# Optimization experiments

Measured on AMD Instinct MI355X. Metric: run time of the kernel, lower is better.

## Reference

```python
import jax, jax.numpy as jnp
import numpy as np

D_MODEL, EDGE_DIM, HIDDEN = 128, 9, 256
B, N = 2, 512


def setup_inputs() -> dict:
    key = jax.random.key(0)
    ks = jax.random.split(key, 12)
    s = 0.05
    return {
        "z_prime": jax.random.normal(ks[0], (B, N, D_MODEL), jnp.float32),
        "edge_features": jax.random.normal(ks[1], (N, N, EDGE_DIM), jnp.float32),
        "candidate_edge_mask": jax.random.randint(ks[2], (N, N), 0, 2, jnp.int32),
        # organ head params (in, out) layout
        "Wo1": jax.random.normal(ks[3], (D_MODEL, HIDDEN), jnp.float32) * s,
        "bo1": jnp.zeros((HIDDEN,), jnp.float32),
        "Wo2": jax.random.normal(ks[4], (HIDDEN, 1), jnp.float32) * s,
        "bo2": jnp.zeros((1,), jnp.float32),
        # edge head first linear, split by input blocks [zi | zj | edge_feat]
        "We_i": jax.random.normal(ks[5], (D_MODEL, HIDDEN), jnp.float32) * s,
        "We_j": jax.random.normal(ks[6], (D_MODEL, HIDDEN), jnp.float32) * s,
        "We_e": jax.random.normal(ks[7], (EDGE_DIM, HIDDEN), jnp.float32) * s,
        "be1": jnp.zeros((HIDDEN,), jnp.float32),
        "We2": jax.random.normal(ks[8], (HIDDEN, 1), jnp.float32) * s,
        "be2": jnp.zeros((1,), jnp.float32),
    }


def reference(z_prime, edge_features, candidate_edge_mask,
              Wo1, bo1, Wo2, bo2, We_i, We_j, We_e, be1, We2, be2):
    # organ head: sigmoid(MLP(z)) -> (B, N)
    h_o = jax.nn.relu(jnp.einsum('bnd,dh->bnh', z_prime, Wo1) + bo1)
    organ_susceptibility = jax.nn.sigmoid(
        (jnp.einsum('bnh,ho->bno', h_o, Wo2) + bo2).squeeze(-1))

    # edge head: concat([zi, zj, E]) @ W1 decomposed into per-node/per-edge
    # projections (identical math to the concatenated linear).
    pi = jnp.einsum('bnd,dh->bnh', z_prime, We_i)   # (B, N, H) -> broadcast over j
    pj = jnp.einsum('bnd,dh->bnh', z_prime, We_j)   # (B, N, H) -> broadcast over i
    pe = jnp.einsum('ijd,dh->ijh', edge_features, We_e)  # (N, N, H)
    h = jax.nn.relu(pi[:, :, None, :] + pj[:, None, :, :] + pe[None] + be1)
    edge_prob = jax.nn.sigmoid(
        (jnp.einsum('bijh,ho->bijo', h, We2) + be2).squeeze(-1))
    edge_prob = edge_prob * candidate_edge_mask.astype(edge_prob.dtype)[None]
    return (organ_susceptibility, edge_prob)
```

## Files before the change

kernel.cpp:

```cpp
#include <hip/hip_runtime.h>
#include <math.h>
#include <stdint.h>

#define D_MODEL 128
#define EDGE_DIM 9
#define HIDDEN 256
#define BATCH 2
#define NN 512

typedef _Float16 h2v    __attribute__((ext_vector_type(2)));
typedef __fp16   fp16x2 __attribute__((ext_vector_type(2)));
typedef _Float16 f16x8  __attribute__((ext_vector_type(8)));
typedef float    f32x4  __attribute__((ext_vector_type(4)));

struct H8 { h2v v[4]; };

__device__ __forceinline__ uint32_t h2u(h2v v) { return __builtin_bit_cast(uint32_t, v); }
__device__ __forceinline__ h2v u2h(uint32_t u) { return __builtin_bit_cast(h2v, u); }
__device__ __forceinline__ h2v pkrtz(float a, float b) {
    return __builtin_bit_cast(h2v, __builtin_amdgcn_cvt_pkrtz(a, b));
}
__device__ __forceinline__ h2v relu2(h2v v) {
    h2v z = {(_Float16)0.0f, (_Float16)0.0f};
    return __builtin_elementwise_max(v, z);
}
__device__ __forceinline__ float fdot2(h2v a, h2v b, float c) {
    return __builtin_amdgcn_fdot2(__builtin_bit_cast(fp16x2, a),
                                  __builtin_bit_cast(fp16x2, b), c, false);
}
__device__ __forceinline__ float sigmoidf_(float x) { return 1.f / (1.f + expf(-x)); }
__device__ __forceinline__ uint32_t el(const uint4& u, int k) {
    switch (k) { case 0: return u.x; case 1: return u.y; case 2: return u.z; default: return u.w; }
}

__global__ __launch_bounds__(512) void node_mfma_kernel(
    const float* __restrict__ z,
    const float* __restrict__ Wo1,
    const float* __restrict__ bo1,
    const float* __restrict__ Wo2,
    const float* __restrict__ bo2,
    const float* __restrict__ We_i,
    const float* __restrict__ We_j,
    const float* __restrict__ be1,
    float* __restrict__ organ_out,
    uint32_t* __restrict__ pi_h,
    uint32_t* __restrict__ pj_q)
{
    __shared__ uint32_t Wlds[256][68];
    __shared__ float org_part[32][4];

    const int t    = threadIdx.x;
    const int lane = t & 63;
    const int wave = t >> 6;
    const int rb   = blockIdx.x;
    const int m    = blockIdx.y;

    const float* __restrict__ W = (m == 0) ? Wo1 : (m == 1) ? We_i : We_j;

    for (int idx = t; idx < 64 * 256; idx += 512) {
        const int d2 = idx >> 8;
        const int h  = idx & 255;
        const float wlo = W[(2 * d2) * 256 + h];
        const float whi = W[(2 * d2 + 1) * 256 + h];
        Wlds[h][d2 ^ ((h & 7) << 3)] = h2u(pkrtz(wlo, whi));
    }

    const int rt = wave & 1;
    const int cg = wave >> 1;
    const int kg = lane >> 4;
    const int row = rb * 32 + rt * 16 + (lane & 15);

    f16x8 A[4];
#pragma unroll
    for (int kt = 0; kt < 4; ++kt) {
        const float4 za = *(const float4*)&z[(size_t)row * 128 + kt * 32 + kg * 8];
        const float4 zb = *(const float4*)&z[(size_t)row * 128 + kt * 32 + kg * 8 + 4];
        H8 a;
        a.v[0] = pkrtz(za.x, za.y); a.v[1] = pkrtz(za.z, za.w);
        a.v[2] = pkrtz(zb.x, zb.y); a.v[3] = pkrtz(zb.z, zb.w);
        A[kt] = __builtin_bit_cast(f16x8, a);
    }

    __syncthreads();

    f32x4 C[4];
#pragma unroll
    for (int ct = 0; ct < 4; ++ct) {
        const int col = (cg * 4 + ct) * 16 + (lane & 15);
        C[ct] = (f32x4){0.f, 0.f, 0.f, 0.f};
#pragma unroll
        for (int kt = 0; kt < 4; ++kt) {
            const int d2b = (kt * 16 + kg * 4) ^ ((col & 7) << 3);
            const uint4 w = *(const uint4*)&Wlds[col][d2b];
            H8 b;
            b.v[0] = u2h(w.x); b.v[1] = u2h(w.y);
            b.v[2] = u2h(w.z); b.v[3] = u2h(w.w);
            C[ct] = __builtin_amdgcn_mfma_f32_16x16x32_f16(
                        A[kt], __builtin_bit_cast(f16x8, b), C[ct], 0, 0, 0);
        }
    }

    if (m == 0) {
        float s0 = 0.f, s1 = 0.f, s2 = 0.f, s3 = 0.f;
#pragma unroll
        for (int ct = 0; ct < 4; ++ct) {
            const int col = (cg * 4 + ct) * 16 + (lane & 15);
            const float b1 = bo1[col];
            const float w2 = Wo2[col];
            s0 = fmaf(fmaxf(C[ct].x + b1, 0.f), w2, s0);
            s1 = fmaf(fmaxf(C[ct].y + b1, 0.f), w2, s1);
            s2 = fmaf(fmaxf(C[ct].z + b1, 0.f), w2, s2);
            s3 = fmaf(fmaxf(C[ct].w + b1, 0.f), w2, s3);
        }
#pragma unroll
        for (int off = 1; off <= 8; off <<= 1) {
            s0 += __shfl_xor(s0, off, 64);
            s1 += __shfl_xor(s1, off, 64);
            s2 += __shfl_xor(s2, off, 64);
            s3 += __shfl_xor(s3, off, 64);
        }
        if ((lane & 15) == 0) {
            const int rbase = rt * 16 + kg * 4;
            org_part[rbase + 0][cg] = s0;
            org_part[rbase + 1][cg] = s1;
            org_part[rbase + 2][cg] = s2;
            org_part[rbase + 3][cg] = s3;
        }
        __syncthreads();
        if (t < 32) {
            const float s = org_part[t][0] + org_part[t][1]
                          + org_part[t][2] + org_part[t][3] + bo2[0];
            organ_out[rb * 32 + t] = sigmoidf_(s);
        }
    } else if (m == 1) {
#pragma unroll
        for (int ct = 0; ct < 4; ++ct) {
            const int col = (cg * 4 + ct) * 16 + (lane & 15);
            const float bv = be1[col];
            float v0 = C[ct].x + bv, v1 = C[ct].y + bv;
            float v2 = C[ct].z + bv, v3 = C[ct].w + bv;
            const float p0 = __shfl_xor(v0, 1, 64);
            const float p1 = __shfl_xor(v1, 1, 64);
            const float p2 = __shfl_xor(v2, 1, 64);
            const float p3 = __shfl_xor(v3, 1, 64);
            if (!(lane & 1)) {
                const int hp = col >> 1;
                const size_t gr = (size_t)(rb * 32 + rt * 16 + kg * 4);
                pi_h[(gr + 0) * 128 + hp] = h2u(pkrtz(v0, p0));
                pi_h[(gr + 1) * 128 + hp] = h2u(pkrtz(v1, p1));
                pi_h[(gr + 2) * 128 + hp] = h2u(pkrtz(v2, p2));
                pi_h[(gr + 3) * 128 + hp] = h2u(pkrtz(v3, p3));
            }
        }
    } else {
#pragma unroll
        for (int ct = 0; ct < 4; ++ct) {
            const int col = (cg * 4 + ct) * 16 + (lane & 15);
            float v0 = C[ct].x, v1 = C[ct].y, v2 = C[ct].z, v3 = C[ct].w;
            const float p0 = __shfl_xor(v0, 1, 64);
            const float p1 = __shfl_xor(v1, 1, 64);
            const float p2 = __shfl_xor(v2, 1, 64);
            const float p3 = __shfl_xor(v3, 1, 64);
            if (!(lane & 1)) {
                const int hp = col >> 1;
                const size_t gr = (size_t)(rb * 32 + rt * 16 + kg * 4);
                const size_t gbase = (size_t)(hp >> 2) * 1024;
                const int    sub   = hp & 3;
                pj_q[(gbase + gr + 0) * 4 + sub] = h2u(pkrtz(v0, p0));
                pj_q[(gbase + gr + 1) * 4 + sub] = h2u(pkrtz(v1, p1));
                pj_q[(gbase + gr + 2) * 4 + sub] = h2u(pkrtz(v2, p2));
                pj_q[(gbase + gr + 3) * 4 + sub] = h2u(pkrtz(v3, p3));
            }
        }
    }
}

__global__ __launch_bounds__(256) void edge_kernel(
    const float* __restrict__ E,
    const int*   __restrict__ mask,
    const float* __restrict__ We_e,
    const float* __restrict__ We2,
    const float* __restrict__ be2,
    const uint32_t* __restrict__ pi_h,
    const uint32_t* __restrict__ pj_q,
    float* __restrict__ edge_out)
{
    __shared__ __align__(16) uint32_t wee_s[EDGE_DIM][128];
    __shared__ __align__(16) uint32_t we2_s[128];
    __shared__ __align__(16) uint32_t pi_s[BATCH][8][128];

    const int t    = threadIdx.x;
    const int lane = t & 63;
    const int w    = t >> 6;
    const int bi   = blockIdx.x;
    const int i0   = (bi >> 4) * 8;
    const int j0   = (bi & 15) * 32;

    const int jl = lane & 31;
    const int ih = lane >> 5;
    const int il = 2 * w + ih;

    for (int idx = t; idx < EDGE_DIM * 128; idx += 256) {
        const int d  = idx >> 7;
        const int h2 = idx & 127;
        wee_s[d][h2] = h2u(pkrtz(We_e[d * 256 + 2 * h2], We_e[d * 256 + 2 * h2 + 1]));
    }
    if (t < 128) we2_s[t] = h2u(pkrtz(We2[2 * t], We2[2 * t + 1]));
#pragma unroll
    for (int k = 0; k < 2; ++k) {
        const int idx = t + k * 256;
        const int r16 = idx >> 5;
        const int c4  = idx & 31;
        const int b   = r16 >> 3;
        const int ii  = r16 & 7;
        const uint4 v = *(const uint4*)&pi_h[(size_t)(b * NN + i0 + ii) * 128 + c4 * 4];
        *(uint4*)&pi_s[b][ii][c4 * 4] = v;
    }

    h2v e[9];
    {
        const float* eptr = &E[((size_t)(i0 + il) * NN + j0 + jl) * EDGE_DIM];
        float ef[9];
#pragma unroll
        for (int d = 0; d < EDGE_DIM; ++d) ef[d] = eptr[d];
#pragma unroll
        for (int d = 0; d < EDGE_DIM; ++d) e[d] = pkrtz(ef[d], ef[d]);
    }

    __syncthreads();

    float acc[2] = {0.f, 0.f};

    const uint4* __restrict__ pjQ = (const uint4*)pj_q;
    const int jrow = j0 + jl;

    uint4 pjn0 = pjQ[jrow];
    uint4 pjn1 = pjQ[NN + jrow];

#pragma unroll 1
    for (int hc = 0; hc < 128; hc += 4) {
        const int g = hc >> 2;
        const uint4 pj40 = pjn0;
        const uint4 pj41 = pjn1;
        if (g < 31) {
            pjn0 = pjQ[(g + 1) * 1024 + jrow];
            pjn1 = pjQ[(g + 1) * 1024 + NN + jrow];
        }
        __builtin_amdgcn_sched_barrier(0);

        uint4 wee4[EDGE_DIM];
#pragma unroll
        for (int d = 0; d < EDGE_DIM; ++d) wee4[d] = *(const uint4*)&wee_s[d][hc];
        const uint4 we24 = *(const uint4*)&we2_s[hc];
        uint4 pi4[2];
        pi4[0] = *(const uint4*)&pi_s[0][il][hc];
        pi4[1] = *(const uint4*)&pi_s[1][il][hc];

#pragma unroll
        for (int k = 0; k < 4; ++k) {
            const h2v w2k = u2h(el(we24, k));
            h2v pe = e[0] * u2h(el(wee4[0], k));
#pragma unroll
            for (int d = 1; d < EDGE_DIM; ++d) pe += e[d] * u2h(el(wee4[d], k));
            h2v t0 = relu2(pe + u2h(el(pj40, k)) + u2h(el(pi4[0], k)));
            acc[0] = fdot2(t0, w2k, acc[0]);
            h2v t1 = relu2(pe + u2h(el(pj41, k)) + u2h(el(pi4[1], k)));
            acc[1] = fdot2(t1, w2k, acc[1]);
        }
    }

    const float b2 = be2[0];
    const int i = i0 + il;
    const float mv = (float)mask[(size_t)i * NN + j0 + jl];
#pragma unroll
    for (int b = 0; b < 2; ++b) {
        const float s = acc[b] + b2;
        edge_out[((size_t)b * NN + i) * NN + j0 + jl] = sigmoidf_(s) * mv;
    }
}

extern "C" void kernel_launch(void* const* d_in, const int* in_sizes, int n_in,
                              void* d_out, int out_size, void* d_ws, size_t ws_size,
                              hipStream_t stream) {
    const float* z    = (const float*)d_in[0];
    const float* E    = (const float*)d_in[1];
    const int*   mask = (const int*)  d_in[2];
    const float* Wo1  = (const float*)d_in[3];
    const float* bo1  = (const float*)d_in[4];
    const float* Wo2  = (const float*)d_in[5];
    const float* bo2  = (const float*)d_in[6];
    const float* We_i = (const float*)d_in[7];
    const float* We_j = (const float*)d_in[8];
    const float* We_e = (const float*)d_in[9];
    const float* be1  = (const float*)d_in[10];
    const float* We2  = (const float*)d_in[11];
    const float* be2  = (const float*)d_in[12];

    float* out_organ = (float*)d_out;
    float* out_edge  = out_organ + BATCH * NN;

    uint32_t* pi_h = (uint32_t*)d_ws;
    uint32_t* pj_q = pi_h + (size_t)BATCH * NN * (HIDDEN/2);

    hipLaunchKernelGGL(node_mfma_kernel,
                       dim3(32, 3), dim3(512), 0, stream,
                       z, Wo1, bo1, Wo2, bo2, We_i, We_j, be1,
                       out_organ, pi_h, pj_q);

    hipLaunchKernelGGL(edge_kernel,
                       dim3(64 * 16), dim3(256), 0, stream,
                       E, mask, We_e, We2, be2, pi_h, pj_q, out_edge);
}
```

Measured before the change: 37.55 us.

## Split edge kernel hidden dimension across waves with shared-memory partial reduction

Each edge block now covers 4 rows of i instead of 8, and the four waves are split into two halves that each handle half of the hidden dimension. The halves combine their partial dot products through shared memory before the sigmoid and mask. This doubles the grid size to raise parallelism and shortens each thread's serial loop. In exchange it recomputes the edge-feature projection per half, adds a barrier and shared-memory reduction, and drops the software prefetch of pj loads.

```diff
diff --git a/kernel.cpp b/kernel.cpp
--- a/kernel.cpp
+++ b/kernel.cpp
@@ -187,18 +187,19 @@
 {
     __shared__ __align__(16) uint32_t wee_s[EDGE_DIM][128];
     __shared__ __align__(16) uint32_t we2_s[128];
-    __shared__ __align__(16) uint32_t pi_s[BATCH][8][128];
+    __shared__ __align__(16) uint32_t pi_s[BATCH][4][128];
+    __shared__ __align__(16) float    part_s[4][32][2];
 
     const int t    = threadIdx.x;
     const int lane = t & 63;
     const int w    = t >> 6;
     const int bi   = blockIdx.x;
-    const int i0   = (bi >> 4) * 8;
+    const int i0   = (bi >> 4) * 4;
     const int j0   = (bi & 15) * 32;
 
     const int jl = lane & 31;
-    const int ih = lane >> 5;
-    const int il = 2 * w + ih;
+    const int il = 2 * (w & 1) + (lane >> 5);
+    const int hh = w >> 1;
 
     for (int idx = t; idx < EDGE_DIM * 128; idx += 256) {
         const int d  = idx >> 7;
@@ -206,13 +207,11 @@
         wee_s[d][h2] = h2u(pkrtz(We_e[d * 256 + 2 * h2], We_e[d * 256 + 2 * h2 + 1]));
     }
     if (t < 128) we2_s[t] = h2u(pkrtz(We2[2 * t], We2[2 * t + 1]));
-#pragma unroll
-    for (int k = 0; k < 2; ++k) {
-        const int idx = t + k * 256;
-        const int r16 = idx >> 5;
-        const int c4  = idx & 31;
-        const int b   = r16 >> 3;
-        const int ii  = r16 & 7;
+    {
+        const int r8 = t >> 5;
+        const int c4 = t & 31;
+        const int b  = r8 >> 2;
+        const int ii = r8 & 3;
         const uint4 v = *(const uint4*)&pi_h[(size_t)(b * NN + i0 + ii) * 128 + c4 * 4];
         *(uint4*)&pi_s[b][ii][c4 * 4] = v;
     }
@@ -233,21 +232,12 @@
 
     const uint4* __restrict__ pjQ = (const uint4*)pj_q;
     const int jrow = j0 + jl;
-
-    uint4 pjn0 = pjQ[jrow];
-    uint4 pjn1 = pjQ[NN + jrow];
+    const int g0   = hh * 16;
 
 #pragma unroll 1
-    for (int hc = 0; hc < 128; hc += 4) {
-        const int g = hc >> 2;
-        const uint4 pj40 = pjn0;
-        const uint4 pj41 = pjn1;
-        if (g < 31) {
-            pjn0 = pjQ[(g + 1) * 1024 + jrow];
-            pjn1 = pjQ[(g + 1) * 1024 + NN + jrow];
-        }
-        __builtin_amdgcn_sched_barrier(0);
-
+    for (int gg = 0; gg < 16; ++gg) {
+        const int g  = g0 + gg;
+        const int hc = g * 4;
         uint4 wee4[EDGE_DIM];
 #pragma unroll
         for (int d = 0; d < EDGE_DIM; ++d) wee4[d] = *(const uint4*)&wee_s[d][hc];
@@ -255,6 +245,8 @@
         uint4 pi4[2];
         pi4[0] = *(const uint4*)&pi_s[0][il][hc];
         pi4[1] = *(const uint4*)&pi_s[1][il][hc];
+        const uint4 pj40 = pjQ[g * 1024 + jrow];
+        const uint4 pj41 = pjQ[g * 1024 + NN + jrow];
 
 #pragma unroll
         for (int k = 0; k < 4; ++k) {
@@ -269,13 +261,19 @@
         }
     }
 
-    const float b2 = be2[0];
-    const int i = i0 + il;
-    const float mv = (float)mask[(size_t)i * NN + j0 + jl];
-#pragma unroll
-    for (int b = 0; b < 2; ++b) {
-        const float s = acc[b] + b2;
-        edge_out[((size_t)b * NN + i) * NN + j0 + jl] = sigmoidf_(s) * mv;
+    if (hh == 1) {
+        part_s[il][jl][0] = acc[0];
+        part_s[il][jl][1] = acc[1];
+    }
+    __syncthreads();
+    if (hh == 0) {
+        const float b2 = be2[0];
+        const int i = i0 + il;
+        const float mv = (float)mask[(size_t)i * NN + j0 + jl];
+        const float s0 = acc[0] + part_s[il][jl][0] + b2;
+        const float s1 = acc[1] + part_s[il][jl][1] + b2;
+        edge_out[((size_t)0 * NN + i) * NN + j0 + jl] = sigmoidf_(s0) * mv;
+        edge_out[((size_t)1 * NN + i) * NN + j0 + jl] = sigmoidf_(s1) * mv;
     }
 }
 
@@ -308,6 +306,6 @@
                        out_organ, pi_h, pj_q);
 
     hipLaunchKernelGGL(edge_kernel,
-                       dim3(64 * 16), dim3(256), 0, stream,
+                       dim3(128 * 16), dim3(256), 0, stream,
                        E, mask, We_e, We2, be2, pi_h, pj_q, out_edge);
 }
```

Result: faster. 35.08 us (-6.6%).
